# Optimization experiments

Measured on AMD Instinct MI355X. Metric: run time of the kernel, lower is better.

Reference implementation:

```python
import jax, jax.numpy as jnp
import numpy as np

B, D, H, W, K = 32, 32, 256, 256, 512
N_TAGS = 30


def setup_inputs() -> dict:
    key = jax.random.key(0)
    k1, k2, k3 = jax.random.split(key, 3)
    ebd_batch = jax.random.normal(k1, (B, D, H, W), dtype=jnp.float32)
    # integer pixel coords (row, col) already in-range -> mask in original is all-true
    kpts = jax.random.randint(k2, (B, K, 2), 0, H).astype(jnp.int64)
    tags = jax.random.randint(k3, (B, K), 0, N_TAGS).astype(jnp.int64)
    return {"ebd_batch": ebd_batch, "kpts": kpts, "tags": tags}


def _per_image(ebd, kp, tg):
    # ebd: [D,H,W], kp: [K,2] int, tg: [K] int
    pred = ebd[:, kp[:, 0], kp[:, 1]]            # [D,K] gathered embeddings
    d = pred.shape[0]
    true_sim = (tg[:, None] == tg[None, :]).astype(pred.dtype)   # [K,K]
    # expo[k,l] = mean_d (pred[d,k]-pred[d,l])^2, via gram expansion (no DxKxK tensor)
    sq = jnp.mean(pred * pred, axis=0)           # [K]
    gram = jnp.einsum('dk,dl->kl', pred, pred) / d
    expo = sq[:, None] + sq[None, :] - 2.0 * gram
    pred_sim = 2.0 / (1.0 + jnp.exp(expo))
    return jnp.mean((true_sim - pred_sim) ** 2)


def reference(ebd_batch, kpts, tags):
    losses = jax.vmap(_per_image)(ebd_batch, kpts, tags)  # [B]
    return jnp.mean(losses)
```

## Files before the change

### kernel.cpp

```cpp
#include <hip/hip_runtime.h>

#define BB 32
#define DD 32
#define HH 256
#define WW 256
#define KK 512

typedef __attribute__((ext_vector_type(8))) short bf16x8;
typedef __attribute__((ext_vector_type(4))) float f32x4;

#define LO_OFF  (1u << 20)
#define SSQ_OFF (2u << 20)

__global__ __launch_bounds__(256) void tagloss_gather(
    const float* __restrict__ ebd, const int* __restrict__ kpts,
    char* __restrict__ ws, float* __restrict__ out) {
  int gid = blockIdx.x * 256 + threadIdx.x;
  if (gid == 0) out[0] = 0.f;
  int col = gid >> 5;
  int d   = gid & 31;
  int b   = col >> 9;

  int y = kpts[col * 2 + 0];
  int x = kpts[col * 2 + 1];
  float v = ebd[((size_t)(b * DD + d)) * (HH * WW) + (size_t)y * WW + x];

  unsigned u  = __float_as_uint(v);
  unsigned rn = u + 0x7FFFu + ((u >> 16) & 1u);
  float hif = __uint_as_float(rn & 0xFFFF0000u);
  float lof = v - hif;
  unsigned ul = __float_as_uint(lof);
  unsigned rl = ul + 0x7FFFu + ((ul >> 16) & 1u);

  ((ushort*)ws)[col * DD + d]            = (ushort)(rn >> 16);
  ((ushort*)(ws + LO_OFF))[col * DD + d] = (ushort)(rl >> 16);

  float s = v * v;
#pragma unroll
  for (int m = 16; m > 0; m >>= 1) s += __shfl_xor(s, m);
  if (d == 0) ((float*)(ws + SSQ_OFF))[col] = s;
}

__global__ __launch_bounds__(256, 2) void tagloss_pairs(
    const char* __restrict__ ws, const int* __restrict__ tags,
    float* __restrict__ out) {
  __shared__ __align__(16) char P[65536];
  __shared__ float ssqL[KK];
  __shared__ int   tagL[KK];
  __shared__ float red[4];

  const int tid = threadIdx.x;
  const int b = blockIdx.y;
  const int slice = blockIdx.x;

#pragma unroll
  for (int i = 0; i < 16; ++i) {
    int j = tid + i * 256;
    int plane = j >> 11;
    int col = (j >> 2) & 511;
    int dc = j & 3;
    const float4* src = (const float4*)(ws + (size_t)plane * LO_OFF +
                                        (size_t)b * 32768 + col * 64 + dc * 16);
    *(float4*)(P + plane * 32768 + col * 64 + ((dc ^ ((col >> 1) & 3)) * 16)) = *src;
  }
  ssqL[tid]       = ((const float*)(ws + SSQ_OFF))[b * KK + tid];
  ssqL[tid + 256] = ((const float*)(ws + SSQ_OFF))[b * KK + tid + 256];
  tagL[tid]       = tags[b * KK + tid];
  tagL[tid + 256] = tags[b * KK + tid + 256];
  __syncthreads();

  const int w = tid >> 6, lane = tid & 63;
  const int lx = lane & 15, dchunk = lane >> 4;

  const int colA = slice * 32 + (w & 1) * 16 + lx;
  const int swzA = ((dchunk ^ ((colA >> 1) & 3)) * 16);
  bf16x8 ahi = *(const bf16x8*)(P + colA * 64 + swzA);
  bf16x8 alo = *(const bf16x8*)(P + 32768 + colA * 64 + swzA);

  const int krow = slice * 32 + (w & 1) * 16 + dchunk * 4;
  float ssqk[4];
  int   tagk[4];
#pragma unroll
  for (int r = 0; r < 4; ++r) { ssqk[r] = ssqL[krow + r]; tagk[r] = tagL[krow + r]; }

  float loss = 0.f;
  const int lt0 = (w >> 1) * 16;
#pragma unroll 4
  for (int q = 0; q < 16; ++q) {
    const int colB = (lt0 + q) * 16 + lx;
    const int swzB = ((dchunk ^ ((colB >> 1) & 3)) * 16);
    bf16x8 bhi = *(const bf16x8*)(P + colB * 64 + swzB);
    bf16x8 blo = *(const bf16x8*)(P + 32768 + colB * 64 + swzB);

    f32x4 acc = {0.f, 0.f, 0.f, 0.f};
    acc = __builtin_amdgcn_mfma_f32_16x16x32_bf16(alo, bhi, acc, 0, 0, 0);
    acc = __builtin_amdgcn_mfma_f32_16x16x32_bf16(ahi, blo, acc, 0, 0, 0);
    acc = __builtin_amdgcn_mfma_f32_16x16x32_bf16(ahi, bhi, acc, 0, 0, 0);

    float ssql = ssqL[colB];
    int   tagl = tagL[colB];
#pragma unroll
    for (int r = 0; r < 4; ++r) {
      float expo = (ssqk[r] + ssql - 2.f * acc[r]) * 0.03125f;
      float ps = 2.f * __builtin_amdgcn_rcpf(1.f + __expf(expo));
      float t = (tagk[r] == tagl) ? 1.f : 0.f;
      float df = t - ps;
      loss = fmaf(df, df, loss);
    }
  }

#pragma unroll
  for (int off = 32; off > 0; off >>= 1) loss += __shfl_down(loss, off);
  if (lane == 0) red[w] = loss;
  __syncthreads();
  if (tid == 0)
    atomicAdd(out, (red[0] + red[1] + red[2] + red[3]) * (1.f / 8388608.f));
}

extern "C" void kernel_launch(void* const* d_in, const int* in_sizes, int n_in,
                              void* d_out, int out_size, void* d_ws, size_t ws_size,
                              hipStream_t stream) {
  const float* ebd  = (const float*)d_in[0];
  const int*   kpts = (const int*)d_in[1];
  const int*   tags = (const int*)d_in[2];
  float* out = (float*)d_out;

  tagloss_gather<<<(BB * KK * DD) / 256, 256, 0, stream>>>(ebd, kpts, (char*)d_ws, out);
  tagloss_pairs<<<dim3(16, BB), 256, 0, stream>>>((const char*)d_ws, tags, out);
}
```

Baseline: 27.94 us.

## Drop LDS staging in pair kernel, read operands directly from global/L2

The pair kernel no longer copies the whole per-image hi/lo bf16 planes, squared norms and tags into shared memory behind a barrier. Each wave now loads its MFMA operands and per-column scalars straight from the workspace, relying on L1/L2 caching. Blocks grow to 512 threads, so each wave handles half as many column tiles and the loop is fully unrolled. This removes the staging cost and the up-front sync, but it adds redundant global loads and uncoalesced scalar reads.

```diff
diff --git a/kernel.cpp b/kernel.cpp
--- a/kernel.cpp
+++ b/kernel.cpp
@@ -41,64 +41,47 @@
   if (d == 0) ((float*)(ws + SSQ_OFF))[col] = s;
 }
 
-__global__ __launch_bounds__(256, 2) void tagloss_pairs(
+__global__ __launch_bounds__(512, 2) void tagloss_pairs(
     const char* __restrict__ ws, const int* __restrict__ tags,
     float* __restrict__ out) {
-  __shared__ __align__(16) char P[65536];
-  __shared__ float ssqL[KK];
-  __shared__ int   tagL[KK];
-  __shared__ float red[4];
+  __shared__ float red[8];
 
   const int tid = threadIdx.x;
   const int b = blockIdx.y;
   const int slice = blockIdx.x;
-
-#pragma unroll
-  for (int i = 0; i < 16; ++i) {
-    int j = tid + i * 256;
-    int plane = j >> 11;
-    int col = (j >> 2) & 511;
-    int dc = j & 3;
-    const float4* src = (const float4*)(ws + (size_t)plane * LO_OFF +
-                                        (size_t)b * 32768 + col * 64 + dc * 16);
-    *(float4*)(P + plane * 32768 + col * 64 + ((dc ^ ((col >> 1) & 3)) * 16)) = *src;
-  }
-  ssqL[tid]       = ((const float*)(ws + SSQ_OFF))[b * KK + tid];
-  ssqL[tid + 256] = ((const float*)(ws + SSQ_OFF))[b * KK + tid + 256];
-  tagL[tid]       = tags[b * KK + tid];
-  tagL[tid + 256] = tags[b * KK + tid + 256];
-  __syncthreads();
-
   const int w = tid >> 6, lane = tid & 63;
   const int lx = lane & 15, dchunk = lane >> 4;
 
+  const char*  hiP  = ws + (size_t)b * 32768;
+  const char*  loP  = ws + LO_OFF + (size_t)b * 32768;
+  const float* ssqB = (const float*)(ws + SSQ_OFF) + b * KK;
+  const int*   tagB = tags + b * KK;
+
   const int colA = slice * 32 + (w & 1) * 16 + lx;
-  const int swzA = ((dchunk ^ ((colA >> 1) & 3)) * 16);
-  bf16x8 ahi = *(const bf16x8*)(P + colA * 64 + swzA);
-  bf16x8 alo = *(const bf16x8*)(P + 32768 + colA * 64 + swzA);
+  bf16x8 ahi = *(const bf16x8*)(hiP + colA * 64 + dchunk * 16);
+  bf16x8 alo = *(const bf16x8*)(loP + colA * 64 + dchunk * 16);
 
   const int krow = slice * 32 + (w & 1) * 16 + dchunk * 4;
   float ssqk[4];
   int   tagk[4];
 #pragma unroll
-  for (int r = 0; r < 4; ++r) { ssqk[r] = ssqL[krow + r]; tagk[r] = tagL[krow + r]; }
+  for (int r = 0; r < 4; ++r) { ssqk[r] = ssqB[krow + r]; tagk[r] = tagB[krow + r]; }
 
   float loss = 0.f;
-  const int lt0 = (w >> 1) * 16;
-#pragma unroll 4
-  for (int q = 0; q < 16; ++q) {
+  const int lt0 = (w >> 1) * 8;
+#pragma unroll
+  for (int q = 0; q < 8; ++q) {
     const int colB = (lt0 + q) * 16 + lx;
-    const int swzB = ((dchunk ^ ((colB >> 1) & 3)) * 16);
-    bf16x8 bhi = *(const bf16x8*)(P + colB * 64 + swzB);
-    bf16x8 blo = *(const bf16x8*)(P + 32768 + colB * 64 + swzB);
+    bf16x8 bhi = *(const bf16x8*)(hiP + colB * 64 + dchunk * 16);
+    bf16x8 blo = *(const bf16x8*)(loP + colB * 64 + dchunk * 16);
 
     f32x4 acc = {0.f, 0.f, 0.f, 0.f};
     acc = __builtin_amdgcn_mfma_f32_16x16x32_bf16(alo, bhi, acc, 0, 0, 0);
     acc = __builtin_amdgcn_mfma_f32_16x16x32_bf16(ahi, blo, acc, 0, 0, 0);
     acc = __builtin_amdgcn_mfma_f32_16x16x32_bf16(ahi, bhi, acc, 0, 0, 0);
 
-    float ssql = ssqL[colB];
-    int   tagl = tagL[colB];
+    float ssql = ssqB[colB];
+    int   tagl = tagB[colB];
 #pragma unroll
     for (int r = 0; r < 4; ++r) {
       float expo = (ssqk[r] + ssql - 2.f * acc[r]) * 0.03125f;
@@ -113,8 +96,12 @@
   for (int off = 32; off > 0; off >>= 1) loss += __shfl_down(loss, off);
   if (lane == 0) red[w] = loss;
   __syncthreads();
-  if (tid == 0)
-    atomicAdd(out, (red[0] + red[1] + red[2] + red[3]) * (1.f / 8388608.f));
+  if (tid == 0) {
+    float s = 0.f;
+#pragma unroll
+    for (int i = 0; i < 8; ++i) s += red[i];
+    atomicAdd(out, s * (1.f / 8388608.f));
+  }
 }
 
 extern "C" void kernel_launch(void* const* d_in, const int* in_sizes, int n_in,
@@ -126,5 +113,5 @@
   float* out = (float*)d_out;
 
   tagloss_gather<<<(BB * KK * DD) / 256, 256, 0, stream>>>(ebd, kpts, (char*)d_ws, out);
-  tagloss_pairs<<<dim3(16, BB), 256, 0, stream>>>((const char*)d_ws, tags, out);
+  tagloss_pairs<<<dim3(16, BB), 512, 0, stream>>>((const char*)d_ws, tags, out);
 }
```

Result: slower. 29.26 us (+4.7%).

## Exploit pair-similarity symmetry by computing only upper-triangular tiles with balanced pairing

Applied to the files above, without the earlier changes.

The pair kernel now computes only the upper-triangular 16x16 tiles of the symmetric KxK similarity matrix. Off-diagonal tiles are weighted by two and diagonal tiles by one. Each block takes row tile p together with row tile 31-p, so every block gets 33 tiles, and the four waves share them round-robin. This roughly halves the MFMA and exp work, but the loop bounds become irregular and the per-job weight adds a little per-iteration overhead.

```diff
diff --git a/kernel.cpp b/kernel.cpp
--- a/kernel.cpp
+++ b/kernel.cpp
@@ -51,7 +51,7 @@
 
   const int tid = threadIdx.x;
   const int b = blockIdx.y;
-  const int slice = blockIdx.x;
+  const int p = blockIdx.x;
 
 #pragma unroll
   for (int i = 0; i < 16; ++i) {
@@ -72,42 +72,62 @@
   const int w = tid >> 6, lane = tid & 63;
   const int lx = lane & 15, dchunk = lane >> 4;
 
-  const int colA = slice * 32 + (w & 1) * 16 + lx;
-  const int swzA = ((dchunk ^ ((colA >> 1) & 3)) * 16);
-  bf16x8 ahi = *(const bf16x8*)(P + colA * 64 + swzA);
-  bf16x8 alo = *(const bf16x8*)(P + 32768 + colA * 64 + swzA);
+  const int i0 = p, i1 = 31 - p;
+  const int lim = 32 - i0;
 
-  const int krow = slice * 32 + (w & 1) * 16 + dchunk * 4;
-  float ssqk[4];
-  int   tagk[4];
+  const int colA0 = i0 * 16 + lx;
+  const int colA1 = i1 * 16 + lx;
+  const int swzA0 = ((dchunk ^ ((colA0 >> 1) & 3)) * 16);
+  const int swzA1 = ((dchunk ^ ((colA1 >> 1) & 3)) * 16);
+  bf16x8 a0hi = *(const bf16x8*)(P + colA0 * 64 + swzA0);
+  bf16x8 a0lo = *(const bf16x8*)(P + 32768 + colA0 * 64 + swzA0);
+  bf16x8 a1hi = *(const bf16x8*)(P + colA1 * 64 + swzA1);
+  bf16x8 a1lo = *(const bf16x8*)(P + 32768 + colA1 * 64 + swzA1);
+
+  const int krow0 = i0 * 16 + dchunk * 4;
+  const int krow1 = i1 * 16 + dchunk * 4;
+  float ssqk0[4], ssqk1[4];
+  int   tagk0[4], tagk1[4];
 #pragma unroll
-  for (int r = 0; r < 4; ++r) { ssqk[r] = ssqL[krow + r]; tagk[r] = tagL[krow + r]; }
+  for (int r = 0; r < 4; ++r) {
+    ssqk0[r] = ssqL[krow0 + r]; tagk0[r] = tagL[krow0 + r];
+    ssqk1[r] = ssqL[krow1 + r]; tagk1[r] = tagL[krow1 + r];
+  }
 
   float loss = 0.f;
-  const int lt0 = (w >> 1) * 16;
-#pragma unroll 4
-  for (int q = 0; q < 16; ++q) {
-    const int colB = (lt0 + q) * 16 + lx;
-    const int swzB = ((dchunk ^ ((colB >> 1) & 3)) * 16);
-    bf16x8 bhi = *(const bf16x8*)(P + colB * 64 + swzB);
-    bf16x8 blo = *(const bf16x8*)(P + 32768 + colB * 64 + swzB);
 
-    f32x4 acc = {0.f, 0.f, 0.f, 0.f};
-    acc = __builtin_amdgcn_mfma_f32_16x16x32_bf16(alo, bhi, acc, 0, 0, 0);
-    acc = __builtin_amdgcn_mfma_f32_16x16x32_bf16(ahi, blo, acc, 0, 0, 0);
-    acc = __builtin_amdgcn_mfma_f32_16x16x32_bf16(ahi, bhi, acc, 0, 0, 0);
+#define JOB(AHI, ALO, SSQK, TAGK, KT, JT)                                      \
+  {                                                                            \
+    const int colB = (JT) * 16 + lx;                                           \
+    const int swzB = ((dchunk ^ ((colB >> 1) & 3)) * 16);                      \
+    bf16x8 bhi = *(const bf16x8*)(P + colB * 64 + swzB);                       \
+    bf16x8 blo = *(const bf16x8*)(P + 32768 + colB * 64 + swzB);               \
+    f32x4 acc = {0.f, 0.f, 0.f, 0.f};                                          \
+    acc = __builtin_amdgcn_mfma_f32_16x16x32_bf16(ALO, bhi, acc, 0, 0, 0);     \
+    acc = __builtin_amdgcn_mfma_f32_16x16x32_bf16(AHI, blo, acc, 0, 0, 0);     \
+    acc = __builtin_amdgcn_mfma_f32_16x16x32_bf16(AHI, bhi, acc, 0, 0, 0);     \
+    float ssql = ssqL[colB];                                                   \
+    int   tagl = tagL[colB];                                                   \
+    float jobLoss = 0.f;                                                       \
+    _Pragma("unroll")                                                          \
+    for (int r = 0; r < 4; ++r) {                                              \
+      float expo = (SSQK[r] + ssql - 2.f * acc[r]) * 0.03125f;                 \
+      float ps = 2.f * __builtin_amdgcn_rcpf(1.f + __expf(expo));              \
+      float t = (TAGK[r] == tagl) ? 1.f : 0.f;                                 \
+      float df = t - ps;                                                       \
+      jobLoss = fmaf(df, df, jobLoss);                                         \
+    }                                                                          \
+    float wtf = ((KT) == (JT)) ? 1.f : 2.f;                                    \
+    loss = fmaf(jobLoss, wtf, loss);                                           \
+  }
 
-    float ssql = ssqL[colB];
-    int   tagl = tagL[colB];
-#pragma unroll
-    for (int r = 0; r < 4; ++r) {
-      float expo = (ssqk[r] + ssql - 2.f * acc[r]) * 0.03125f;
-      float ps = 2.f * __builtin_amdgcn_rcpf(1.f + __expf(expo));
-      float t = (tagk[r] == tagl) ? 1.f : 0.f;
-      float df = t - ps;
-      loss = fmaf(df, df, loss);
-    }
+  for (int t = w; t < lim; t += 4) JOB(a0hi, a0lo, ssqk0, tagk0, i0, i0 + t);
+  {
+    int m0 = (lim > w) ? ((lim - w + 3) >> 2) : 0;
+    for (int t = w + 4 * m0; t < 33; t += 4)
+      JOB(a1hi, a1lo, ssqk1, tagk1, i1, i1 + (t - lim));
   }
+#undef JOB
 
 #pragma unroll
   for (int off = 32; off > 0; off >>= 1) loss += __shfl_down(loss, off);
```

After: 27.35 us. -2.1%, faster.
